# Performance work log

Measured on AMD Instinct MI355X. Metric: run time of the kernel, lower is better.

## Reference

```python
import jax, jax.numpy as jnp
import numpy as np

D = 128   # per-head dim
H = 16    # num heads
B = 2
S = 2048

def setup_inputs() -> dict:
    key = jax.random.key(0)
    ks = jax.random.split(key, 9)
    DH = D * H
    sc_in = 1.0 / np.sqrt(D)
    sc_dh = 1.0 / np.sqrt(DH)
    return {
        "x": jax.random.normal(ks[0], (B, S, D), jnp.float32),
        "Wq": jax.random.uniform(ks[1], (D, DH), jnp.float32, -sc_in, sc_in),
        "bq": jax.random.uniform(ks[2], (DH,), jnp.float32, -sc_in, sc_in),
        "Wk": jax.random.uniform(ks[3], (D, DH), jnp.float32, -sc_in, sc_in),
        "bk": jax.random.uniform(ks[4], (DH,), jnp.float32, -sc_in, sc_in),
        "Wv": jax.random.uniform(ks[5], (D, DH), jnp.float32, -sc_in, sc_in),
        "bv": jax.random.uniform(ks[6], (DH,), jnp.float32, -sc_in, sc_in),
        "Wo": jax.random.uniform(ks[7], (DH, D), jnp.float32, -sc_dh, sc_dh),
        "bo": jax.random.uniform(ks[8], (D,), jnp.float32, -sc_dh, sc_dh),
    }

def reference(x, Wq, bq, Wk, bk, Wv, bv, Wo, bo):
    Bx, Sx, _ = x.shape
    def split(t):  # (B,S,D*H) -> (B,H,S,D)
        return t.reshape(Bx, Sx, H, D).transpose(0, 2, 1, 3)
    Q = split(x @ Wq + bq)
    K = split(x @ Wk + bk)
    V = split(x @ Wv + bv)
    scores = jnp.einsum('bhsd,bhtd->bhst', Q, K) / jnp.sqrt(jnp.float32(D))
    weights = jax.nn.softmax(scores, axis=-1)
    out = jnp.einsum('bhst,bhtd->bhsd', weights, V)  # (B,H,S,D)
    out = out.transpose(0, 2, 1, 3).reshape(Bx, Sx, H * D)
    return out @ Wo + bo
```

## Files before the change

### kernel.cpp

```cpp
#include <hip/hip_runtime.h>
#include <cstdint>
#include <cstddef>

typedef __bf16 bf16_t;
typedef bf16_t bf16x8 __attribute__((ext_vector_type(8)));
typedef bf16_t bf16x4 __attribute__((ext_vector_type(4)));
typedef float  f32x4  __attribute__((ext_vector_type(4)));

#define MFMA16(a, b, c) __builtin_amdgcn_mfma_f32_16x16x32_bf16((a), (b), (c), 0, 0, 0)

#define GLOAD16(GP, LP)                                                           \
    __builtin_amdgcn_global_load_lds(                                             \
        (const __attribute__((address_space(1))) unsigned int*)(GP),              \
        (__attribute__((address_space(3))) unsigned int*)(LP), 16, 0, 0)

static constexpr int Bb = 2, Ss = 2048, Hh = 16, Dd = 128, DH = 2048;
static constexpr float QSCALE = 0.08838834764831845f * 1.4426950408889634f;

__global__ __launch_bounds__(256) void k_prep(
    const float* __restrict__ x,
    const float* __restrict__ Wq, const float* __restrict__ Wk,
    const float* __restrict__ Wv, const float* __restrict__ Wo,
    bf16_t* __restrict__ xb, bf16_t* __restrict__ Wt, bf16_t* __restrict__ Wot) {
    __shared__ float t[32][33];
    const int tid = threadIdx.x;
    const int bid = blockIdx.x;
    if (bid < 512) {
        int i = (bid * 256 + tid) * 4;
        float4 v = *reinterpret_cast<const float4*>(x + i);
        bf16x4 o;
        o[0] = (bf16_t)v.x; o[1] = (bf16_t)v.y; o[2] = (bf16_t)v.z; o[3] = (bf16_t)v.w;
        *reinterpret_cast<bf16x4*>(xb + i) = o;
        return;
    }
    const int u = bid - 512, m = u >> 8, tt = u & 255;
    const float* src; bf16_t* dst; int R, C, bx, by;
    if (m < 3) { src = (m == 0) ? Wq : (m == 1) ? Wk : Wv; dst = Wt + (size_t)m * 262144;
                 R = 128;  C = 2048; bx = tt & 63, by = tt >> 6; }
    else       { src = Wo; dst = Wot;
                 R = 2048; C = 128;  bx = tt & 3,  by = tt >> 2; }
    const int tx = tid & 31, ty = tid >> 5;
    const int c0 = bx * 32, r0 = by * 32;
#pragma unroll
    for (int i = 0; i < 4; i++)
        t[ty + i * 8][tx] = src[(size_t)(r0 + ty + i * 8) * C + c0 + tx];
    __syncthreads();
#pragma unroll
    for (int i = 0; i < 4; i++)
        dst[(size_t)(c0 + ty + i * 8) * R + r0 + tx] = (bf16_t)t[tx][ty + i * 8];
}

__global__ __launch_bounds__(256) void k_qkv(
    const bf16_t* __restrict__ xb, const bf16_t* __restrict__ Wt,
    const float* __restrict__ bq, const float* __restrict__ bk, const float* __restrict__ bv,
    bf16_t* __restrict__ Qw, bf16_t* __restrict__ Kw, bf16_t* __restrict__ Vw) {
    __shared__ bf16_t smem[17408];
    bf16_t* Bs = smem;

    const int tid = threadIdx.x;
    const int w = tid >> 6, lane = tid & 63, c = lane & 15, g = lane >> 4;
    const int cm = c & 7;
    const int m0 = blockIdx.x * 128, n0g = blockIdx.y * 128, z = blockIdx.z;
    const bf16_t* Wz = Wt + (size_t)z * DH * Dd;
    const int wm = w * 32;

#pragma unroll
    for (int i = 0; i < 8; i++) {
        int e = tid + i * 256; int row = e >> 4, bg = e & 15;
        *reinterpret_cast<uint4*>(&Bs[row * 128 + ((bg ^ (row & 7)) * 8)]) =
            *reinterpret_cast<const uint4*>(&Wz[(size_t)(n0g + row) * 128 + bg * 8]);
    }
    __syncthreads();

    f32x4 acc[2][8];
#pragma unroll
    for (int a = 0; a < 2; a++)
#pragma unroll
        for (int b = 0; b < 8; b++) acc[a][b] = f32x4{0.f, 0.f, 0.f, 0.f};

    const int ar0 = m0 + wm + c;
#pragma unroll
    for (int kb = 0; kb < 4; kb++) {
        bf16x8 af0 = *reinterpret_cast<const bf16x8*>(&xb[(size_t)ar0 * 128 + kb * 32 + g * 8]);
        bf16x8 af1 = *reinterpret_cast<const bf16x8*>(&xb[(size_t)(ar0 + 16) * 128 + kb * 32 + g * 8]);
#pragma unroll
        for (int nb = 0; nb < 8; nb++) {
            bf16x8 bfr = *reinterpret_cast<const bf16x8*>(
                &Bs[(nb * 16 + c) * 128 + (((4 * kb + g) ^ cm) * 8)]);
            acc[0][nb] = MFMA16(af0, bfr, acc[0][nb]);
            acc[1][nb] = MFMA16(af1, bfr, acc[1][nb]);
        }
    }

    const float* bias = (z == 0) ? bq : (z == 1) ? bk : bv;
    const float sc = (z == 0) ? QSCALE : 1.0f;
    const int cstride = (z == 2) ? 131 : 136;
    __syncthreads();
#pragma unroll
    for (int mb = 0; mb < 2; mb++)
#pragma unroll
        for (int nb = 0; nb < 8; nb++) {
            float bs = bias[n0g + nb * 16 + c];
#pragma unroll
            for (int r = 0; r < 4; r++) {
                int row = wm + mb * 16 + g * 4 + r;
                int col = nb * 16 + c;
                smem[row * cstride + col] = (bf16_t)((acc[mb][nb][r] + bs) * sc);
            }
        }
    __syncthreads();
    const int h = blockIdx.y;
    if (z <= 1) {
        bf16_t* O = z ? Kw : Qw;
#pragma unroll
        for (int i = 0; i < 8; i++) {
            int e = tid + i * 256; int row = e >> 4, col = (e & 15) * 8;
            int sg = m0 + row, b = sg >> 11, s2 = sg & 2047;
            *reinterpret_cast<uint4*>(&O[(((size_t)(b * Hh + h)) * Ss + s2) * Dd + col]) =
                *reinterpret_cast<const uint4*>(&smem[row * 136 + col]);
        }
    } else {
        int b = m0 >> 11; int sbase = m0 & 2047;
        const unsigned short* cs16 = reinterpret_cast<const unsigned short*>(smem);
#pragma unroll
        for (int i = 0; i < 32; i++) {
            int e = tid + i * 256; int d = e >> 6, sl2 = (e & 63) * 2;
            unsigned int lo = cs16[sl2 * 131 + d], hi = cs16[(sl2 + 1) * 131 + d];
            unsigned int pk = lo | (hi << 16);
            *reinterpret_cast<unsigned int*>(
                &Vw[(((size_t)(b * Hh + h)) * Dd + d) * Ss + sbase + sl2]) = pk;
        }
    }
}

#define SOFTMAX_HALF(SACC, M_RUN, L_RUN, AO, PROW)                                   \
    do {                                                                             \
        float pm = fmaxf(fmaxf(SACC[0][0], SACC[0][1]), fmaxf(SACC[0][2], SACC[0][3])); \
        _Pragma("unroll")                                                            \
        for (int nb = 1; nb < 4; nb++)                                               \
            _Pragma("unroll")                                                        \
            for (int r = 0; r < 4; r++) pm = fmaxf(pm, SACC[nb][r]);                 \
        pm = fmaxf(pm, __shfl_xor(pm, 16));                                          \
        pm = fmaxf(pm, __shfl_xor(pm, 32));                                          \
        if (!__all(pm <= M_RUN + 11.5f)) {                                           \
            float mn_ = fmaxf(M_RUN, pm);                                            \
            float sc_ = exp2f(M_RUN - mn_);                                          \
            M_RUN = mn_;                                                             \
            L_RUN *= sc_;                                                            \
            _Pragma("unroll")                                                        \
            for (int r = 0; r < 4; r++) {                                            \
                float s4_ = __shfl(sc_, g * 4 + r);                                  \
                _Pragma("unroll")                                                    \
                for (int db = 0; db < 8; db++) AO[db][r] *= s4_;                     \
            }                                                                        \
        }                                                                            \
        float rs_ = 0.f;                                                             \
        _Pragma("unroll")                                                            \
        for (int nb = 0; nb < 4; nb++) {                                             \
            bf16x4 pk_;                                                              \
            _Pragma("unroll")                                                        \
            for (int r = 0; r < 4; r++) {                                            \
                float pe_ = exp2f(SACC[nb][r] - M_RUN);                              \
                rs_ += pe_;                                                          \
                pk_[r] = (bf16_t)pe_;                                                \
            }                                                                        \
            *reinterpret_cast<bf16x4*>(                                              \
                &PbF[(PROW) * 64 + (((2 * nb + (g >> 1)) ^ cm) * 8) + (g & 1) * 4]) = pk_; \
        }                                                                            \
        L_RUN += rs_;                                                                \
    } while (0)

__global__ __launch_bounds__(256, 2) void k_attn(
    const bf16_t* __restrict__ Qw, const bf16_t* __restrict__ Kw,
    const bf16_t* __restrict__ Vw, bf16_t* __restrict__ AO) {
    __shared__ bf16_t smem[32768];
    bf16_t* KtF0 = smem;
    bf16_t* KtF1 = smem + 8192;
    bf16_t* VtF  = smem + 16384;
    bf16_t* PbF  = smem + 24576;

    const int tid = threadIdx.x;
    const int w = tid >> 6, lane = tid & 63, c = lane & 15, g = lane >> 4;
    const int cm = c & 7;

    const int f = blockIdx.x;
    const int wid = (f & 7) * 64 + (f >> 3);
    const int bh = wid >> 4, q0 = (wid & 15) * 128;

    const bf16_t* Qb = Qw + (size_t)bh * Ss * Dd;
    const bf16_t* Kb = Kw + (size_t)bh * Ss * Dd;
    const bf16_t* Vb = Vw + (size_t)bh * Dd * Ss;

    bf16x8 qlo[4], qhi[4];
    const int qrl = q0 + w * 32 + c, qrh = qrl + 16;
#pragma unroll
    for (int kb = 0; kb < 4; kb++) {
        qlo[kb] = *reinterpret_cast<const bf16x8*>(&Qb[(size_t)qrl * Dd + kb * 32 + g * 8]);
        qhi[kb] = *reinterpret_cast<const bf16x8*>(&Qb[(size_t)qrh * Dd + kb * 32 + g * 8]);
    }

    f32x4 aolo[8], aohi[8];
#pragma unroll
    for (int i = 0; i < 8; i++) { aolo[i] = f32x4{0.f,0.f,0.f,0.f}; aohi[i] = f32x4{0.f,0.f,0.f,0.f}; }
    float m_lo = -1e30f, l_lo = 0.f, m_hi = -1e30f, l_hi = 0.f;

    const int krl = lane >> 4;
    const int kc0 = ((lane & 15) ^ krl) * 8;
    const bf16_t* ke = Kb + (w * 16 + krl) * 128 + kc0;
    const bf16_t* ko = Kb + (w * 16 + krl) * 128 + (kc0 ^ 32);
    const int vrl = lane >> 3;
    const int vc0 = ((lane & 7) ^ vrl) * 8;
    const bf16_t* vsrc = Vb + (w * 32 + vrl) * 2048 + vc0;

    const unsigned wq = __builtin_amdgcn_readfirstlane((unsigned)(w * 2048));
    bf16_t* kd0 = KtF0 + wq;
    bf16_t* kd1 = KtF1 + wq;
    bf16_t* vd  = VtF  + wq;

    GLOAD16(ke,        kd0);
    GLOAD16(ko + 512,  kd0 + 512);
    GLOAD16(ke + 1024, kd0 + 1024);
    GLOAD16(ko + 1536, kd0 + 1536);
    ke += 8192; ko += 8192;
    asm volatile("s_waitcnt vmcnt(0)" ::: "memory");
    __syncthreads();

    for (int t = 0; t < 32; ++t) {
        GLOAD16(vsrc,         vd);
        GLOAD16(vsrc + 16384, vd + 512);
        GLOAD16(vsrc + 32768, vd + 1024);
        GLOAD16(vsrc + 49152, vd + 1536);
        vsrc += 64;

        const bf16_t* kr = (t & 1) ? KtF1 : KtF0;
        f32x4 slo[4], shi[4];
#pragma unroll
        for (int nb = 0; nb < 4; nb++) { slo[nb] = f32x4{0.f,0.f,0.f,0.f}; shi[nb] = f32x4{0.f,0.f,0.f,0.f}; }
        __builtin_amdgcn_s_setprio(1);
#pragma unroll
        for (int kb = 0; kb < 4; kb++)
#pragma unroll
            for (int nb = 0; nb < 4; nb++) {
                bf16x8 kf = *reinterpret_cast<const bf16x8*>(
                    &kr[(nb * 16 + c) * 128 + ((4 * kb + g) ^ cm) * 8]);
                slo[nb] = MFMA16(kf, qlo[kb], slo[nb]);
                shi[nb] = MFMA16(kf, qhi[kb], shi[nb]);
            }
        __builtin_amdgcn_s_setprio(0);

        SOFTMAX_HALF(slo, m_lo, l_lo, aolo, w * 32 + c);
        SOFTMAX_HALF(shi, m_hi, l_hi, aohi, w * 32 + 16 + c);

        asm volatile("s_waitcnt vmcnt(0)" ::: "memory");
        __syncthreads();

        if (t < 31) {
            bf16_t* kd = (t & 1) ? kd0 : kd1;
            GLOAD16(ke,        kd);
            GLOAD16(ko + 512,  kd + 512);
            GLOAD16(ke + 1024, kd + 1024);
            GLOAD16(ko + 1536, kd + 1536);
            ke += 8192; ko += 8192;
        }

        bf16x8 plo[2], phi[2];
#pragma unroll
        for (int kb2 = 0; kb2 < 2; kb2++) {
            plo[kb2] = *reinterpret_cast<const bf16x8*>(
                &PbF[(w * 32 + c) * 64 + ((4 * kb2 + g) ^ cm) * 8]);
            phi[kb2] = *reinterpret_cast<const bf16x8*>(
                &PbF[(w * 32 + 16 + c) * 64 + ((4 * kb2 + g) ^ cm) * 8]);
        }
        __builtin_amdgcn_s_setprio(1);
#pragma unroll
        for (int db = 0; db < 8; db++)
#pragma unroll
            for (int kb2 = 0; kb2 < 2; kb2++) {
                bf16x8 vf = *reinterpret_cast<const bf16x8*>(
                    &VtF[(db * 16 + c) * 64 + ((4 * kb2 + g) ^ cm) * 8]);
                aolo[db] = MFMA16(plo[kb2], vf, aolo[db]);
                aohi[db] = MFMA16(phi[kb2], vf, aohi[db]);
            }
        __builtin_amdgcn_s_setprio(0);

        asm volatile("s_waitcnt vmcnt(0)" ::: "memory");
        __syncthreads();
    }

    l_lo += __shfl_xor(l_lo, 16); l_lo += __shfl_xor(l_lo, 32);
    l_hi += __shfl_xor(l_hi, 16); l_hi += __shfl_xor(l_hi, 32);
    float ilo = 1.0f / l_lo, ihi = 1.0f / l_hi;
    bf16_t (*Os)[136] = reinterpret_cast<bf16_t(*)[136]>(smem);
#pragma unroll
    for (int r = 0; r < 4; r++) {
        float i4l = __shfl(ilo, g * 4 + r);
        float i4h = __shfl(ihi, g * 4 + r);
        int rowl = w * 32 + g * 4 + r, rowh = rowl + 16;
#pragma unroll
        for (int db = 0; db < 8; db++) {
            Os[rowl][db * 16 + c] = (bf16_t)(aolo[db][r] * i4l);
            Os[rowh][db * 16 + c] = (bf16_t)(aohi[db][r] * i4h);
        }
    }
    __syncthreads();
    const int b = bh >> 4, h = bh & 15;
#pragma unroll
    for (int i = 0; i < 8; i++) {
        int e = tid + i * 256; int row = e >> 4, col = (e & 15) * 8;
        *reinterpret_cast<uint4*>(&AO[((size_t)(b * Ss + q0 + row)) * DH + h * Dd + col]) =
            *reinterpret_cast<const uint4*>(&Os[row][col]);
    }
}

__global__ __launch_bounds__(256) void k_outproj(
    const bf16_t* __restrict__ A, const bf16_t* __restrict__ Wot,
    const float* __restrict__ bo, float* __restrict__ out) {
    const int tid = threadIdx.x;
    const int w = tid >> 6, lane = tid & 63, c = lane & 15, g = lane >> 4;
    const int mt = blockIdx.x >> 1, nh = blockIdx.x & 1;
    const int m0 = mt * 16;
    const int nb = nh * 4 + w;

    f32x4 a0 = f32x4{0.f,0.f,0.f,0.f}, a1 = f32x4{0.f,0.f,0.f,0.f};
    f32x4 a2 = f32x4{0.f,0.f,0.f,0.f}, a3 = f32x4{0.f,0.f,0.f,0.f};

    const bf16_t* Ab = A   + (size_t)(m0 + c) * DH + g * 8;
    const bf16_t* Bw = Wot + (size_t)(nb * 16 + c) * DH + g * 8;

#pragma unroll 4
    for (int kk = 0; kk < 64; kk += 4) {
        bf16x8 af0  = *reinterpret_cast<const bf16x8*>(Ab + (kk + 0) * 32);
        bf16x8 bf0  = *reinterpret_cast<const bf16x8*>(Bw + (kk + 0) * 32);
        bf16x8 af1  = *reinterpret_cast<const bf16x8*>(Ab + (kk + 1) * 32);
        bf16x8 bf1  = *reinterpret_cast<const bf16x8*>(Bw + (kk + 1) * 32);
        bf16x8 af2  = *reinterpret_cast<const bf16x8*>(Ab + (kk + 2) * 32);
        bf16x8 bf2  = *reinterpret_cast<const bf16x8*>(Bw + (kk + 2) * 32);
        bf16x8 af3  = *reinterpret_cast<const bf16x8*>(Ab + (kk + 3) * 32);
        bf16x8 bf3  = *reinterpret_cast<const bf16x8*>(Bw + (kk + 3) * 32);
        a0 = MFMA16(af0, bf0, a0);
        a1 = MFMA16(af1, bf1, a1);
        a2 = MFMA16(af2, bf2, a2);
        a3 = MFMA16(af3, bf3, a3);
    }

    f32x4 acc = (a0 + a1) + (a2 + a3);

    float bs = bo[nb * 16 + c];
#pragma unroll
    for (int r = 0; r < 4; r++)
        out[(size_t)(m0 + g * 4 + r) * Dd + nb * 16 + c] = acc[r] + bs;
}

extern "C" void kernel_launch(void* const* d_in, const int* in_sizes, int n_in,
                              void* d_out, int out_size, void* d_ws, size_t ws_size,
                              hipStream_t stream) {
    const float* x  = (const float*)d_in[0];
    const float* Wq = (const float*)d_in[1];
    const float* bq = (const float*)d_in[2];
    const float* Wk = (const float*)d_in[3];
    const float* bk = (const float*)d_in[4];
    const float* Wv = (const float*)d_in[5];
    const float* bv = (const float*)d_in[6];
    const float* Wo = (const float*)d_in[7];
    const float* bo = (const float*)d_in[8];
    float* out = (float*)d_out;

    char* ws = (char*)d_ws;
    bf16_t* xb  = (bf16_t*)(ws);
    bf16_t* Wt  = (bf16_t*)(ws + 1048576);
    bf16_t* Wot = (bf16_t*)(ws + 2621440);
    bf16_t* Qw  = (bf16_t*)(ws + 3145728);
    bf16_t* Kw  = (bf16_t*)(ws + 3145728 + 16777216);
    bf16_t* Vw  = (bf16_t*)(ws + 3145728 + 2 * 16777216);
    bf16_t* AO  = (bf16_t*)(ws + 3145728 + 3 * 16777216);

    k_prep<<<1536, 256, 0, stream>>>(x, Wq, Wk, Wv, Wo, xb, Wt, Wot);
    k_qkv<<<dim3(32, 16, 3), 256, 0, stream>>>(xb, Wt, bq, bk, bv, Qw, Kw, Vw);
    k_attn<<<512, 256, 0, stream>>>(Qw, Kw, Vw, AO);
    k_outproj<<<512, 256, 0, stream>>>(AO, Wot, bo, out);
}
```

Measured before the change: 145.1 us.

## Single-buffer K tile via register prefetch to fit three blocks per CU

Replaces the double-buffered K tile in LDS, filled by direct global-to-LDS loads, with a single K buffer. The next K tile is prefetched into registers during compute and written to LDS after the mid-iteration barrier. This cuts shared memory per block from 64KB to 48KB, and launch bounds are raised to 3 blocks per CU for more occupancy. The risks are higher register pressure under the tighter bound, possible spills, and the removed explicit vmcnt waits, which could leave the V global-to-LDS loads unordered before the barrier.

```diff
diff --git a/kernel.cpp b/kernel.cpp
--- a/kernel.cpp
+++ b/kernel.cpp
@@ -170,14 +170,13 @@
         L_RUN += rs_;                                                                \
     } while (0)
 
-__global__ __launch_bounds__(256, 2) void k_attn(
+__global__ __launch_bounds__(256, 3) void k_attn(
     const bf16_t* __restrict__ Qw, const bf16_t* __restrict__ Kw,
     const bf16_t* __restrict__ Vw, bf16_t* __restrict__ AO) {
-    __shared__ bf16_t smem[32768];
-    bf16_t* KtF0 = smem;
-    bf16_t* KtF1 = smem + 8192;
-    bf16_t* VtF  = smem + 16384;
-    bf16_t* PbF  = smem + 24576;
+    __shared__ bf16_t smem[24576];
+    bf16_t* KtF = smem;
+    bf16_t* VtF = smem + 8192;
+    bf16_t* PbF = smem + 16384;
 
     const int tid = threadIdx.x;
     const int w = tid >> 6, lane = tid & 63, c = lane & 15, g = lane >> 4;
@@ -204,25 +203,31 @@
     for (int i = 0; i < 8; i++) { aolo[i] = f32x4{0.f,0.f,0.f,0.f}; aohi[i] = f32x4{0.f,0.f,0.f,0.f}; }
     float m_lo = -1e30f, l_lo = 0.f, m_hi = -1e30f, l_hi = 0.f;
 
-    const int krl = lane >> 4;
-    const int kc0 = ((lane & 15) ^ krl) * 8;
-    const bf16_t* ke = Kb + (w * 16 + krl) * 128 + kc0;
-    const bf16_t* ko = Kb + (w * 16 + krl) * 128 + (kc0 ^ 32);
+    const int krow = lane >> 4;
+    const int kcb  = lane & 15;
+    const bf16_t* ksrc = Kb + (w * 16 + krow) * 128 + kcb * 8;
+    bf16_t* kd0 = KtF + (w * 16 + krow +  0) * 128 + ((kcb ^ ( krow      & 7)) * 8);
+    bf16_t* kd1 = KtF + (w * 16 + krow +  4) * 128 + ((kcb ^ ((krow + 4) & 7)) * 8);
+    bf16_t* kd2 = KtF + (w * 16 + krow +  8) * 128 + ((kcb ^ ( krow      & 7)) * 8);
+    bf16_t* kd3 = KtF + (w * 16 + krow + 12) * 128 + ((kcb ^ ((krow + 4) & 7)) * 8);
+
     const int vrl = lane >> 3;
     const int vc0 = ((lane & 7) ^ vrl) * 8;
     const bf16_t* vsrc = Vb + (w * 32 + vrl) * 2048 + vc0;
-
     const unsigned wq = __builtin_amdgcn_readfirstlane((unsigned)(w * 2048));
-    bf16_t* kd0 = KtF0 + wq;
-    bf16_t* kd1 = KtF1 + wq;
-    bf16_t* vd  = VtF  + wq;
-
-    GLOAD16(ke,        kd0);
-    GLOAD16(ko + 512,  kd0 + 512);
-    GLOAD16(ke + 1024, kd0 + 1024);
-    GLOAD16(ko + 1536, kd0 + 1536);
-    ke += 8192; ko += 8192;
-    asm volatile("s_waitcnt vmcnt(0)" ::: "memory");
+    bf16_t* vd = VtF + wq;
+
+    {
+        uint4 k0 = *reinterpret_cast<const uint4*>(ksrc);
+        uint4 k1 = *reinterpret_cast<const uint4*>(ksrc + 512);
+        uint4 k2 = *reinterpret_cast<const uint4*>(ksrc + 1024);
+        uint4 k3 = *reinterpret_cast<const uint4*>(ksrc + 1536);
+        *reinterpret_cast<uint4*>(kd0) = k0;
+        *reinterpret_cast<uint4*>(kd1) = k1;
+        *reinterpret_cast<uint4*>(kd2) = k2;
+        *reinterpret_cast<uint4*>(kd3) = k3;
+        ksrc += 8192;
+    }
     __syncthreads();
 
     for (int t = 0; t < 32; ++t) {
@@ -231,8 +236,15 @@
         GLOAD16(vsrc + 32768, vd + 1024);
         GLOAD16(vsrc + 49152, vd + 1536);
         vsrc += 64;
-
-        const bf16_t* kr = (t & 1) ? KtF1 : KtF0;
+        uint4 kp0, kp1, kp2, kp3;
+        if (t < 31) {
+            kp0 = *reinterpret_cast<const uint4*>(ksrc);
+            kp1 = *reinterpret_cast<const uint4*>(ksrc + 512);
+            kp2 = *reinterpret_cast<const uint4*>(ksrc + 1024);
+            kp3 = *reinterpret_cast<const uint4*>(ksrc + 1536);
+            ksrc += 8192;
+        }
+
         f32x4 slo[4], shi[4];
 #pragma unroll
         for (int nb = 0; nb < 4; nb++) { slo[nb] = f32x4{0.f,0.f,0.f,0.f}; shi[nb] = f32x4{0.f,0.f,0.f,0.f}; }
@@ -242,7 +254,7 @@
 #pragma unroll
             for (int nb = 0; nb < 4; nb++) {
                 bf16x8 kf = *reinterpret_cast<const bf16x8*>(
-                    &kr[(nb * 16 + c) * 128 + ((4 * kb + g) ^ cm) * 8]);
+                    &KtF[(nb * 16 + c) * 128 + ((4 * kb + g) ^ cm) * 8]);
                 slo[nb] = MFMA16(kf, qlo[kb], slo[nb]);
                 shi[nb] = MFMA16(kf, qhi[kb], shi[nb]);
             }
@@ -251,16 +263,13 @@
         SOFTMAX_HALF(slo, m_lo, l_lo, aolo, w * 32 + c);
         SOFTMAX_HALF(shi, m_hi, l_hi, aohi, w * 32 + 16 + c);
 
-        asm volatile("s_waitcnt vmcnt(0)" ::: "memory");
         __syncthreads();
 
         if (t < 31) {
-            bf16_t* kd = (t & 1) ? kd0 : kd1;
-            GLOAD16(ke,        kd);
-            GLOAD16(ko + 512,  kd + 512);
-            GLOAD16(ke + 1024, kd + 1024);
-            GLOAD16(ko + 1536, kd + 1536);
-            ke += 8192; ko += 8192;
+            *reinterpret_cast<uint4*>(kd0) = kp0;
+            *reinterpret_cast<uint4*>(kd1) = kp1;
+            *reinterpret_cast<uint4*>(kd2) = kp2;
+            *reinterpret_cast<uint4*>(kd3) = kp3;
         }
 
         bf16x8 plo[2], phi[2];
@@ -283,7 +292,6 @@
             }
         __builtin_amdgcn_s_setprio(0);
 
-        asm volatile("s_waitcnt vmcnt(0)" ::: "memory");
         __syncthreads();
     }
 
```

After: 180.2 us. 24.2% more time.
